# Kernel optimization log

Hardware: AMD Instinct MI355X
Metric: run time of the kernel (lower is better)

The kernel has to match this reference:

```python
import jax, jax.numpy as jnp
import numpy as np

DIM = 768
HEADS = 12
K_PARTS = 64
MLP_HIDDEN = 4 * DIM
EPS = 1e-5


def layer_norm(x, g, b):
    mu = jnp.mean(x, axis=-1, keepdims=True)
    var = jnp.mean(jnp.square(x - mu), axis=-1, keepdims=True)
    return (x - mu) * jax.lax.rsqrt(var + EPS) * g + b


def attention(x, qkv_w, qkv_b, proj_w, proj_b, num_heads):
    B, N, C = x.shape
    hd = C // num_heads
    scale = hd ** -0.5
    qkv = x @ qkv_w.T + qkv_b                      # (B,N,3C)
    qkv = qkv.reshape(B, N, 3, num_heads, hd).transpose(2, 0, 3, 1, 4)  # (3,B,H,N,hd)
    q, k, v = qkv[0], qkv[1], qkv[2]
    attn = jax.nn.softmax(jnp.einsum('bhqd,bhkd->bhqk', q, k) * scale, axis=-1)
    out = jnp.einsum('bhqk,bhkd->bhqd', attn, v)   # (B,H,N,hd)
    out = out.transpose(0, 2, 1, 3).reshape(B, N, C)
    return out @ proj_w.T + proj_b, attn


def mlp(x, fc1_w, fc1_b, fc2_w, fc2_b):
    h = jax.nn.gelu(x @ fc1_w.T + fc1_b, approximate=False)
    return h @ fc2_w.T + fc2_b


def setup_inputs() -> dict:
    key = jax.random.key(0)
    ks = jax.random.split(key, 16)
    s = lambda fan_in: 1.0 / np.sqrt(fan_in)
    inp = {
        'x': jax.random.normal(ks[0], (8, 1024, DIM), dtype=jnp.float32),
        'ln1_g': jnp.ones((DIM,), jnp.float32),
        'ln1_b': jnp.zeros((DIM,), jnp.float32),
        'qkv_w': jax.random.normal(ks[1], (3 * DIM, DIM), jnp.float32) * s(DIM),
        'qkv_b': jnp.zeros((3 * DIM,), jnp.float32),
        'proj_w': jax.random.normal(ks[2], (DIM, DIM), jnp.float32) * s(DIM),
        'proj_b': jnp.zeros((DIM,), jnp.float32),
        'c_qkv_w': jax.random.normal(ks[3], (3 * DIM, DIM), jnp.float32) * s(DIM),
        'c_qkv_b': jnp.zeros((3 * DIM,), jnp.float32),
        'c_proj_w': jax.random.normal(ks[4], (DIM, DIM), jnp.float32) * s(DIM),
        'c_proj_b': jnp.zeros((DIM,), jnp.float32),
        'cp_fc1_w': jax.random.normal(ks[5], (K_PARTS, K_PARTS), jnp.float32) * s(K_PARTS),
        'cp_fc1_b': jnp.zeros((K_PARTS,), jnp.float32),
        'cp_fc2_w': jax.random.normal(ks[6], (DIM, K_PARTS), jnp.float32) * s(K_PARTS),
        'cp_fc2_b': jnp.zeros((DIM,), jnp.float32),
        'P': jax.random.normal(ks[7], (K_PARTS, DIM), jnp.float32),
        'ln2_g': jnp.ones((DIM,), jnp.float32),
        'ln2_b': jnp.zeros((DIM,), jnp.float32),
        'fc1_w': jax.random.normal(ks[8], (MLP_HIDDEN, DIM), jnp.float32) * s(DIM),
        'fc1_b': jnp.zeros((MLP_HIDDEN,), jnp.float32),
        'fc2_w': jax.random.normal(ks[9], (DIM, MLP_HIDDEN), jnp.float32) * s(MLP_HIDDEN),
        'fc2_b': jnp.zeros((DIM,), jnp.float32),
    }
    # normalize P rows like the module init (F.normalize(orthogonal, dim=-1))
    inp['P'] = inp['P'] / jnp.linalg.norm(inp['P'], axis=-1, keepdims=True)
    return inp


def reference(x, ln1_g, ln1_b, qkv_w, qkv_b, proj_w, proj_b,
              c_qkv_w, c_qkv_b, c_proj_w, c_proj_b,
              cp_fc1_w, cp_fc1_b, cp_fc2_w, cp_fc2_b, P,
              ln2_g, ln2_b, fc1_w, fc1_b, fc2_w, fc2_b):
    n1 = layer_norm(x, ln1_g, ln1_b)
    y, _ = attention(n1, qkv_w, qkv_b, proj_w, proj_b, HEADS)
    # SimilarityMaps: L2-normalize tokens and parts, cosine similarity map (B,N,K)
    Un = n1 / jnp.linalg.norm(n1, axis=-1, keepdims=True)
    Pn = P / jnp.linalg.norm(P, axis=-1, keepdims=True)
    dmap = jnp.einsum('bnd,kd->bnk', Un, Pn)
    # c_project: Mlp K -> K -> dim, then parts attention
    zin = mlp(dmap, cp_fc1_w, cp_fc1_b, cp_fc2_w, cp_fc2_b)
    z, _ = attention(zin, c_qkv_w, c_qkv_b, c_proj_w, c_proj_b, HEADS)
    x = x + y + z                                  # gamma_1 is None, drop_path=0
    x = x + mlp(layer_norm(x, ln2_g, ln2_b), fc1_w, fc1_b, fc2_w, fc2_b)
    return x, dmap
```

## Files before the change

### kernel.cpp

```cpp
#include <hip/hip_runtime.h>


typedef unsigned short u16;
typedef unsigned int   u32;
typedef __attribute__((ext_vector_type(8))) short short8;
typedef __attribute__((ext_vector_type(8))) unsigned short ushort8v;
typedef __attribute__((ext_vector_type(4))) float f32x4;

#define F_GELU     1
#define F_ROWSCALE 2
#define F_RES1     4
#define F_RESF     8
#define F_OUTB     16
#define F_OUTF     32
#define F_BIAS     64

__device__ __forceinline__ float bf2f(u32 b) { return __uint_as_float(b << 16); }
__device__ __forceinline__ u16 f2bf(float f) {
    u32 u = __float_as_uint(f);
    u32 r = u + 0x7fffu + ((u >> 16) & 1u);
    return (u16)(r >> 16);
}
__device__ __forceinline__ u16 f2bf_fast(float f) {
    return (u16)((__float_as_uint(f) + 0x8000u) >> 16);
}
__device__ __forceinline__ float gelu_exact(float v) {
    return 0.5f * v * (1.0f + erff(v * 0.70710678118654752440f));
}
__device__ __forceinline__ float gelu_fast(float x) {
    float u = 0.79788456080286535588f * (x + 0.044715f * x * x * x);
    float e = __builtin_amdgcn_exp2f(u * 2.88539008177792681472f);
    float t = 1.0f - 2.0f / (e + 1.0f);
    return 0.5f * x * (1.0f + t);
}

__device__ __forceinline__ void gload16(const u16* g, u16* l) {
    __builtin_amdgcn_global_load_lds(
        (const __attribute__((address_space(1))) u32*)g,
        (__attribute__((address_space(3))) u32*)l, 16, 0, 0);
}

__global__ __launch_bounds__(256)
void conv_k(const float* __restrict__ src, u16* __restrict__ dst, int n)
{
    const int base = (blockIdx.x * 256 + threadIdx.x) * 4;
    if (base >= n) return;
    float4 v = *(const float4*)(src + base);
    ushort4 o;
    o.x = f2bf(v.x); o.y = f2bf(v.y); o.z = f2bf(v.z); o.w = f2bf(v.w);
    *(ushort4*)(dst + base) = o;
}

__device__ __forceinline__ float block_sum(float v, float* red) {
    #pragma unroll
    for (int off = 32; off > 0; off >>= 1) v += __shfl_down(v, off);
    __syncthreads();
    if ((threadIdx.x & 63) == 0) red[threadIdx.x >> 6] = v;
    __syncthreads();
    return red[0] + red[1] + red[2] + red[3];
}

template<bool NORM>
__global__ __launch_bounds__(256)
void ln_k(const float* __restrict__ xin, const float* __restrict__ g,
          const float* __restrict__ bta, u16* __restrict__ out,
          float* __restrict__ invnorm)
{
    __shared__ float red[4];
    const int row = blockIdx.x, t = threadIdx.x;
    float v[3];
    #pragma unroll
    for (int i = 0; i < 3; i++)
        v[i] = xin[(size_t)row * 768 + t + i * 256];
    float tot = block_sum(v[0] + v[1] + v[2], red);
    float mu  = tot * (1.0f / 768.0f);
    float d0 = v[0] - mu, d1 = v[1] - mu, d2 = v[2] - mu;
    float tot2 = block_sum(d0 * d0 + d1 * d1 + d2 * d2, red);
    float rstd = rsqrtf(tot2 * (1.0f / 768.0f) + 1e-5f);
    float ss = 0.0f;
    #pragma unroll
    for (int i = 0; i < 3; i++) {
        int c = t + i * 256;
        float yy = (v[i] - mu) * rstd * g[c] + bta[c];
        out[(size_t)row * 768 + c] = f2bf(yy);
        ss += yy * yy;
    }
    if constexpr (NORM) {
        float tot3 = block_sum(ss, red);
        if (t == 0) invnorm[row] = rsqrtf(tot3);
    }
}

__global__ __launch_bounds__(256)
void pn_k(const float* __restrict__ P, u16* __restrict__ Pn)
{
    __shared__ float red[4];
    const int row = blockIdx.x, t = threadIdx.x;
    float v[3];
    #pragma unroll
    for (int i = 0; i < 3; i++)
        v[i] = P[(size_t)row * 768 + t + i * 256];
    float tot = block_sum(v[0]*v[0] + v[1]*v[1] + v[2]*v[2], red);
    float inv = rsqrtf(tot);
    #pragma unroll
    for (int i = 0; i < 3; i++)
        Pn[(size_t)row * 768 + t + i * 256] = f2bf(v[i] * inv);
}

template<int FLAGS>
__global__ __launch_bounds__(256)
void gemm_mfma(const u16* __restrict__ A, const u16* __restrict__ W,
               const float* __restrict__ bias,
               const u16* __restrict__ res1, const float* __restrict__ resf,
               u16* __restrict__ out, float* __restrict__ outf,
               int M, int N, int K)
{
    __shared__ u16 smem[3][8192];
    const int t = threadIdx.x;
    const int wave = t >> 6, lane = t & 63;
    const int nbx  = gridDim.x;
    const int orig = blockIdx.x + blockIdx.y * nbx;
    const int cpx  = (nbx * gridDim.y) >> 3;
    const int wg   = (orig & 7) * cpx + (orig >> 3);
    const int m0 = (wg / nbx) * 128, n0 = (wg % nbx) * 128;
    const int Wm = (wave >> 1) * 64, Wn = (wave & 1) * 64;
    const int rr = lane >> 2, cc = (lane & 3) * 8;
    const int quad = lane >> 4, r16 = lane & 15;
    const int NK = K >> 5;

    f32x4 acc[4][4];
    #pragma unroll
    for (int i = 0; i < 4; i++)
        #pragma unroll
        for (int j = 0; j < 4; j++)
            acc[i][j] = (f32x4){0.f, 0.f, 0.f, 0.f};

    #pragma unroll
    for (int c = 0; c < 2; c++) {
        const int chunk = wave * 2 + c;
        const int row = chunk * 16 + rr;
        gload16(A + (size_t)(m0 + row) * K + cc, &smem[0][chunk * 512]);
        gload16(W + (size_t)(n0 + row) * K + cc, &smem[0][4096 + chunk * 512]);
    }
    if (NK > 1) {
        #pragma unroll
        for (int c = 0; c < 2; c++) {
            const int chunk = wave * 2 + c;
            const int row = chunk * 16 + rr;
            gload16(A + (size_t)(m0 + row) * K + 32 + cc, &smem[1][chunk * 512]);
            gload16(W + (size_t)(n0 + row) * K + 32 + cc, &smem[1][4096 + chunk * 512]);
        }
    }

    for (int kt = 0; kt < NK; kt++) {
        const int cur = kt % 3;
        if (kt + 2 < NK) {
            const int k0 = (kt + 2) * 32;
            const int nb = (kt + 2) % 3;
            #pragma unroll
            for (int c = 0; c < 2; c++) {
                const int chunk = wave * 2 + c;
                const int row = chunk * 16 + rr;
                gload16(A + (size_t)(m0 + row) * K + k0 + cc,
                        &smem[nb][chunk * 512]);
                gload16(W + (size_t)(n0 + row) * K + k0 + cc,
                        &smem[nb][4096 + chunk * 512]);
            }
            asm volatile("s_waitcnt vmcnt(8)\n\ts_barrier" ::: "memory");
        } else if (kt + 1 < NK) {
            asm volatile("s_waitcnt vmcnt(4)\n\ts_barrier" ::: "memory");
        } else {
            asm volatile("s_waitcnt vmcnt(0)\n\ts_barrier" ::: "memory");
        }
        short8 af[4], bfr[4];
        #pragma unroll
        for (int i = 0; i < 4; i++) {
            af[i]  = *(const short8*)&smem[cur][(Wm + i * 16 + r16) * 32 + quad * 8];
            bfr[i] = *(const short8*)&smem[cur][4096 + (Wn + i * 16 + r16) * 32 + quad * 8];
        }
        #pragma unroll
        for (int i = 0; i < 4; i++)
            #pragma unroll
            for (int j = 0; j < 4; j++)
                acc[i][j] = __builtin_amdgcn_mfma_f32_16x16x32_bf16(
                    af[i], bfr[j], acc[i][j], 0, 0, 0);
        asm volatile("s_barrier" ::: "memory");
    }

    float* myl = (float*)&smem[0][0] + wave * 1088;
    float bj[4];
    #pragma unroll
    for (int j = 0; j < 4; j++) {
        if constexpr (FLAGS & F_BIAS) bj[j] = bias[n0 + Wn + j * 16 + r16];
        else bj[j] = 0.0f;
    }
    const int row = lane >> 2, seg = (lane & 3) * 16;

    #pragma unroll
    for (int i = 0; i < 4; i++) {
        #pragma unroll
        for (int j = 0; j < 4; j++)
            #pragma unroll
            for (int r = 0; r < 4; r++) {
                float v = acc[i][j][r] + bj[j];
                if constexpr (FLAGS & F_GELU) v = gelu_fast(v);
                myl[(quad * 4 + r) * 68 + j * 16 + r16] = v;
            }
        float v[16];
        #pragma unroll
        for (int k4 = 0; k4 < 4; k4++) {
            float4 f = *(const float4*)&myl[row * 68 + seg + k4 * 4];
            v[k4 * 4 + 0] = f.x; v[k4 * 4 + 1] = f.y;
            v[k4 * 4 + 2] = f.z; v[k4 * 4 + 3] = f.w;
        }
        const int m = m0 + Wm + i * 16 + row;
        const size_t idx = (size_t)m * N + n0 + Wn + seg;
        if constexpr (FLAGS & F_RES1) {
            ushort8v r0 = *(const ushort8v*)(res1 + idx);
            ushort8v r1 = *(const ushort8v*)(res1 + idx + 8);
            #pragma unroll
            for (int k = 0; k < 8; k++) { v[k] += bf2f(r0[k]); v[k + 8] += bf2f(r1[k]); }
        }
        if constexpr (FLAGS & F_RESF) {
            #pragma unroll
            for (int k4 = 0; k4 < 4; k4++) {
                float4 f = *(const float4*)(resf + idx + k4 * 4);
                v[k4 * 4 + 0] += f.x; v[k4 * 4 + 1] += f.y;
                v[k4 * 4 + 2] += f.z; v[k4 * 4 + 3] += f.w;
            }
        }
        if constexpr (FLAGS & F_OUTB) {
            ushort8v o0, o1;
            #pragma unroll
            for (int k = 0; k < 8; k++) { o0[k] = f2bf(v[k]); o1[k] = f2bf(v[k + 8]); }
            *(ushort8v*)(out + idx) = o0;
            *(ushort8v*)(out + idx + 8) = o1;
        }
        if constexpr (FLAGS & F_OUTF) {
            #pragma unroll
            for (int k4 = 0; k4 < 4; k4++) {
                float4 f = {v[k4 * 4 + 0], v[k4 * 4 + 1], v[k4 * 4 + 2], v[k4 * 4 + 3]};
                *(float4*)(outf + idx + k4 * 4) = f;
            }
        }
    }
}

template<int BM, int BN, int FLAGS>
__global__ __launch_bounds__(256)
void gemm_k(const u16* __restrict__ A, const u16* __restrict__ W,
            const float* __restrict__ bias, const float* __restrict__ rowscale,
            const u16* __restrict__ res1, const float* __restrict__ resf,
            u16* __restrict__ out, float* __restrict__ outf,
            int M, int N, int K)
{
    constexpr int RM = BM / 16, RN = BN / 16;
    __shared__ float Asm[16][BM + 4];
    __shared__ float Wsm[16][BN + 4];
    const int t  = threadIdx.x;
    const int tx = t & 15, ty = t >> 4;
    const int m0 = blockIdx.y * BM, n0 = blockIdx.x * BN;

    float acc[RM][RN];
    #pragma unroll
    for (int i = 0; i < RM; i++)
        #pragma unroll
        for (int j = 0; j < RN; j++) acc[i][j] = 0.0f;

    for (int k0 = 0; k0 < K; k0 += 16) {
        #pragma unroll
        for (int i = 0; i < BM / 64; i++) {
            int f = t + i * 256, r = f >> 2, c4 = (f & 3) << 2;
            uint2 u = *(const uint2*)(A + (size_t)(m0 + r) * K + k0 + c4);
            Asm[c4 + 0][r] = bf2f(u.x & 0xffffu);
            Asm[c4 + 1][r] = bf2f(u.x >> 16);
            Asm[c4 + 2][r] = bf2f(u.y & 0xffffu);
            Asm[c4 + 3][r] = bf2f(u.y >> 16);
        }
        #pragma unroll
        for (int i = 0; i < BN / 64; i++) {
            int f = t + i * 256, r = f >> 2, c4 = (f & 3) << 2;
            uint2 u = *(const uint2*)(W + (size_t)(n0 + r) * K + k0 + c4);
            Wsm[c4 + 0][r] = bf2f(u.x & 0xffffu);
            Wsm[c4 + 1][r] = bf2f(u.x >> 16);
            Wsm[c4 + 2][r] = bf2f(u.y & 0xffffu);
            Wsm[c4 + 3][r] = bf2f(u.y >> 16);
        }
        __syncthreads();
        #pragma unroll
        for (int k = 0; k < 16; k++) {
            float a[RM], w[RN];
            #pragma unroll
            for (int ii = 0; ii < RM; ii += 4) {
                float4 v = *(const float4*)&Asm[k][ty * RM + ii];
                a[ii] = v.x; a[ii + 1] = v.y; a[ii + 2] = v.z; a[ii + 3] = v.w;
            }
            #pragma unroll
            for (int jj = 0; jj < RN; jj += 4) {
                float4 v = *(const float4*)&Wsm[k][tx * RN + jj];
                w[jj] = v.x; w[jj + 1] = v.y; w[jj + 2] = v.z; w[jj + 3] = v.w;
            }
            #pragma unroll
            for (int i = 0; i < RM; i++)
                #pragma unroll
                for (int j = 0; j < RN; j++)
                    acc[i][j] = fmaf(a[i], w[j], acc[i][j]);
        }
        __syncthreads();
    }

    #pragma unroll
    for (int i = 0; i < RM; i++) {
        const int m = m0 + ty * RM + i;
        float rs = 1.0f;
        if constexpr (FLAGS & F_ROWSCALE) rs = rowscale[m];
        #pragma unroll
        for (int jj = 0; jj < RN; jj += 4) {
            const int n = n0 + tx * RN + jj;
            const size_t idx = (size_t)m * N + n;
            float b4[4] = {0.f, 0.f, 0.f, 0.f};
            if constexpr (FLAGS & F_BIAS) {
                float4 bvv = *(const float4*)(bias + n);
                b4[0] = bvv.x; b4[1] = bvv.y; b4[2] = bvv.z; b4[3] = bvv.w;
            }
            float e[4];
            #pragma unroll
            for (int j = 0; j < 4; j++) {
                float v = acc[i][jj + j];
                if constexpr (FLAGS & F_BIAS) v += b4[j];
                if constexpr (FLAGS & F_GELU) v = gelu_exact(v);
                if constexpr (FLAGS & F_ROWSCALE) v *= rs;
                e[j] = v;
            }
            if constexpr (FLAGS & F_OUTB) {
                ushort4 o4;
                o4.x = f2bf(e[0]); o4.y = f2bf(e[1]);
                o4.z = f2bf(e[2]); o4.w = f2bf(e[3]);
                *(ushort4*)(out + idx) = o4;
            }
            if constexpr (FLAGS & F_OUTF) {
                float4 o4 = {e[0], e[1], e[2], e[3]};
                *(float4*)(outf + idx) = o4;
            }
        }
    }
}

__global__ __launch_bounds__(256)
void attn_mfma(const u16* __restrict__ qkv, u16* __restrict__ out)
{
    const int orig = blockIdx.x + blockIdx.y * 8;
    const int wg   = (orig & 7) * 96 + (orig >> 3);
    const int qt = wg & 7;
    const int bh = wg >> 3;
    const int b = bh / 12, h = bh % 12;
    __shared__ u16 Qs[2 * 128 * 32];
    __shared__ u16 Ks[2 * 64 * 32];
    __shared__ u16 Vt[2 * 64 * 32];
    __shared__ u16 Ps[2 * 128 * 32];
    const int t = threadIdx.x;
    const int wave = t >> 6, lane = t & 63;
    const int quad = lane >> 4, r16 = lane & 15;
    const size_t RS = 2304;
    const int tok0 = b * 1024 + qt * 128;
    const u16* qbase = qkv + (size_t)tok0 * RS + h * 64;
    const float SC = 0.125f * 1.44269504088896340736f;

    #pragma unroll
    for (int c = 0; c < 4; c++) {
        int idx = wave * 4 + c;
        int kc = idx >> 3, rg = idx & 7;
        int row = rg * 16 + (lane >> 2);
        gload16(qbase + (size_t)row * RS + kc * 32 + (lane & 3) * 8,
                &Qs[kc * 4096 + rg * 512]);
    }

    f32x4 O[2][4];
    float lpart[2][4];
    #pragma unroll
    for (int i = 0; i < 2; i++)
        #pragma unroll
        for (int j = 0; j < 4; j++) {
            O[i][j] = (f32x4){0.f, 0.f, 0.f, 0.f};
            lpart[i][j & 3] = 0.0f;
        }

    for (int kt = 0; kt < 16; kt++) {
        const u16* kbase = qkv + (size_t)(b * 1024 + kt * 64) * RS + 768 + h * 64;
        #pragma unroll
        for (int c = 0; c < 2; c++) {
            int idx = wave * 2 + c;
            int kc = idx >> 2, rg = idx & 3;
            int row = rg * 16 + (lane >> 2);
            gload16(kbase + (size_t)row * RS + kc * 32 + (lane & 3) * 8,
                    &Ks[kc * 2048 + rg * 512]);
        }
        const u16* vbase = qkv + (size_t)(b * 1024 + kt * 64) * RS + 1536 + h * 64;
        {
            const int kp = t & 63, dg = t >> 6;
            const int vb = (kp >> 5) * 2048 + (kp & 31);
            #pragma unroll
            for (int it = 0; it < 4; it++) {
                int d0 = dg * 16 + it * 4;
                uint2 u = *(const uint2*)(vbase + (size_t)kp * RS + d0);
                Vt[vb + (d0 + 0) * 32] = (u16)(u.x & 0xffffu);
                Vt[vb + (d0 + 1) * 32] = (u16)(u.x >> 16);
                Vt[vb + (d0 + 2) * 32] = (u16)(u.y & 0xffffu);
                Vt[vb + (d0 + 3) * 32] = (u16)(u.y >> 16);
            }
        }
        __syncthreads();

        f32x4 S[2][4];
        #pragma unroll
        for (int i = 0; i < 2; i++)
            #pragma unroll
            for (int j = 0; j < 4; j++)
                S[i][j] = (f32x4){0.f, 0.f, 0.f, 0.f};
        __builtin_amdgcn_s_setprio(1);
        #pragma unroll
        for (int kc = 0; kc < 2; kc++) {
            short8 aq[2], bk[4];
            #pragma unroll
            for (int i = 0; i < 2; i++)
                aq[i] = *(const short8*)&Qs[kc * 4096 + (wave * 32 + i * 16 + r16) * 32 + quad * 8];
            #pragma unroll
            for (int j = 0; j < 4; j++)
                bk[j] = *(const short8*)&Ks[kc * 2048 + (j * 16 + r16) * 32 + quad * 8];
            #pragma unroll
            for (int i = 0; i < 2; i++)
                #pragma unroll
                for (int j = 0; j < 4; j++)
                    S[i][j] = __builtin_amdgcn_mfma_f32_16x16x32_bf16(
                        aq[i], bk[j], S[i][j], 0, 0, 0);
        }
        __builtin_amdgcn_s_setprio(0);

        #pragma unroll
        for (int i = 0; i < 2; i++) {
            #pragma unroll
            for (int j = 0; j < 4; j++) {
                const int col = j * 16 + r16;
                const int pb = (col >> 5) * 4096 + (col & 31);
                #pragma unroll
                for (int r = 0; r < 4; r++) {
                    float p = __builtin_amdgcn_exp2f(S[i][j][r] * SC);
                    lpart[i][r] += p;
                    const int row = wave * 32 + i * 16 + quad * 4 + r;
                    Ps[pb + row * 32] = f2bf_fast(p);
                }
            }
        }

        __builtin_amdgcn_s_setprio(1);
        #pragma unroll
        for (int kc = 0; kc < 2; kc++) {
            short8 ap[2], bv[4];
            #pragma unroll
            for (int i = 0; i < 2; i++)
                ap[i] = *(const short8*)&Ps[kc * 4096 + (wave * 32 + i * 16 + r16) * 32 + quad * 8];
            #pragma unroll
            for (int j = 0; j < 4; j++)
                bv[j] = *(const short8*)&Vt[kc * 2048 + (j * 16 + r16) * 32 + quad * 8];
            #pragma unroll
            for (int i = 0; i < 2; i++)
                #pragma unroll
                for (int j = 0; j < 4; j++)
                    O[i][j] = __builtin_amdgcn_mfma_f32_16x16x32_bf16(
                        ap[i], bv[j], O[i][j], 0, 0, 0);
        }
        __builtin_amdgcn_s_setprio(0);
        __syncthreads();
    }

    const int row = lane >> 2, seg = (lane & 3) * 16;
    #pragma unroll
    for (int i = 0; i < 2; i++) {
        float linv[4];
        #pragma unroll
        for (int r = 0; r < 4; r++) {
            float l = lpart[i][r];
            l += __shfl_xor(l, 1);
            l += __shfl_xor(l, 2);
            l += __shfl_xor(l, 4);
            l += __shfl_xor(l, 8);
            linv[r] = 1.0f / l;
        }
        u16* myl = &Ps[wave * 2048 + i * 1024];
        #pragma unroll
        for (int j = 0; j < 4; j++)
            #pragma unroll
            for (int r = 0; r < 4; r++)
                myl[(quad * 4 + r) * 64 + j * 16 + r16] = f2bf(O[i][j][r] * linv[r]);
        const int token = tok0 + wave * 32 + i * 16 + row;
        const size_t oidx = (size_t)token * 768 + h * 64 + seg;
        *(ushort8v*)(out + oidx)     = *(const ushort8v*)&myl[row * 64 + seg];
        *(ushort8v*)(out + oidx + 8) = *(const ushort8v*)&myl[row * 64 + seg + 8];
    }
}

extern "C" void kernel_launch(void* const* d_in, const int* in_sizes, int n_in,
                              void* d_out, int out_size, void* d_ws, size_t ws_size,
                              hipStream_t stream)
{
    (void)in_sizes; (void)n_in; (void)out_size; (void)ws_size;
    const float* x        = (const float*)d_in[0];
    const float* ln1_g    = (const float*)d_in[1];
    const float* ln1_b    = (const float*)d_in[2];
    const float* qkv_w    = (const float*)d_in[3];
    const float* qkv_b    = (const float*)d_in[4];
    const float* proj_w   = (const float*)d_in[5];
    const float* proj_b   = (const float*)d_in[6];
    const float* c_qkv_w  = (const float*)d_in[7];
    const float* c_qkv_b  = (const float*)d_in[8];
    const float* c_proj_w = (const float*)d_in[9];
    const float* c_proj_b = (const float*)d_in[10];
    const float* cp_fc1_w = (const float*)d_in[11];
    const float* cp_fc1_b = (const float*)d_in[12];
    const float* cp_fc2_w = (const float*)d_in[13];
    const float* cp_fc2_b = (const float*)d_in[14];
    const float* P        = (const float*)d_in[15];
    const float* ln2_g    = (const float*)d_in[16];
    const float* ln2_b    = (const float*)d_in[17];
    const float* fc1_w    = (const float*)d_in[18];
    const float* fc1_b    = (const float*)d_in[19];
    const float* fc2_w    = (const float*)d_in[20];
    const float* fc2_b    = (const float*)d_in[21];

    float* out_x    = (float*)d_out;
    float* out_dmap = out_x + 6291456;

    u16* us    = (u16*)d_ws;
    u16* n1n2  = us;
    u16* bigA  = us + 6291456;
    u16* ao    = bigA + 18874368;
    u16* y     = us + 31457280;
    float* xs  = (float*)(us + 37748736);
    u16* dmapb = us + 50331648;
    u16* cph   = us + 50855936;
    u16* Pn    = us + 51380224;
    float* invn = (float*)(us + 51429376);
    u16* ci    = us + 51445760;

    u16* w_qkv   = ci;
    u16* w_proj  = ci + 1769472;
    u16* w_cqkv  = ci + 2359296;
    u16* w_cproj = ci + 4128768;
    u16* w_cpf1  = ci + 4718592;
    u16* w_cpf2  = ci + 4722688;
    u16* w_fc1   = ci + 4771840;
    u16* w_fc2   = ci + 7131136;

    const float* wsrc[8] = { qkv_w, proj_w, c_qkv_w, c_proj_w,
                             cp_fc1_w, cp_fc2_w, fc1_w, fc2_w };
    u16* wdst[8] = { w_qkv, w_proj, w_cqkv, w_cproj,
                     w_cpf1, w_cpf2, w_fc1, w_fc2 };
    const int wn[8] = { 1769472, 589824, 1769472, 589824,
                        4096, 49152, 2359296, 2359296 };
    for (int i = 0; i < 8; i++)
        conv_k<<<(wn[i] / 4 + 255) / 256, 256, 0, stream>>>(wsrc[i], wdst[i], wn[i]);

    pn_k<<<64, 256, 0, stream>>>(P, Pn);
    ln_k<true><<<8192, 256, 0, stream>>>(x, ln1_g, ln1_b, n1n2, invn);
    gemm_mfma<F_BIAS | F_OUTB>
        <<<dim3(18, 64), 256, 0, stream>>>(n1n2, w_qkv, qkv_b, nullptr, nullptr,
                                           bigA, nullptr, 8192, 2304, 768);
    attn_mfma<<<dim3(8, 96), 256, 0, stream>>>(bigA, ao);
    gemm_mfma<F_BIAS | F_OUTB>
        <<<dim3(6, 64), 256, 0, stream>>>(ao, w_proj, proj_b, nullptr, nullptr,
                                          y, nullptr, 8192, 768, 768);
    gemm_k<64, 64, F_ROWSCALE | F_OUTB | F_OUTF>
        <<<dim3(1, 128), 256, 0, stream>>>(n1n2, Pn, nullptr, invn, nullptr,
                                           nullptr, dmapb, out_dmap, 8192, 64, 768);
    gemm_k<64, 64, F_BIAS | F_GELU | F_OUTB>
        <<<dim3(1, 128), 256, 0, stream>>>(dmapb, w_cpf1, cp_fc1_b, nullptr,
                                           nullptr, nullptr, cph, nullptr, 8192, 64, 64);
    gemm_mfma<F_BIAS | F_OUTB>
        <<<dim3(6, 64), 256, 0, stream>>>(cph, w_cpf2, cp_fc2_b, nullptr, nullptr,
                                          n1n2, nullptr, 8192, 768, 64);
    gemm_mfma<F_BIAS | F_OUTB>
        <<<dim3(18, 64), 256, 0, stream>>>(n1n2, w_cqkv, c_qkv_b, nullptr, nullptr,
                                           bigA, nullptr, 8192, 2304, 768);
    attn_mfma<<<dim3(8, 96), 256, 0, stream>>>(bigA, ao);
    gemm_mfma<F_BIAS | F_RES1 | F_RESF | F_OUTF>
        <<<dim3(6, 64), 256, 0, stream>>>(ao, w_cproj, c_proj_b, y, x,
                                          nullptr, xs, 8192, 768, 768);
    ln_k<false><<<8192, 256, 0, stream>>>(xs, ln2_g, ln2_b, n1n2, nullptr);
    gemm_mfma<F_BIAS | F_GELU | F_OUTB>
        <<<dim3(24, 64), 256, 0, stream>>>(n1n2, w_fc1, fc1_b, nullptr, nullptr,
                                           bigA, nullptr, 8192, 3072, 768);
    gemm_mfma<F_BIAS | F_RESF | F_OUTF>
        <<<dim3(6, 64), 256, 0, stream>>>(bigA, w_fc2, fc2_b, nullptr, xs,
                                          nullptr, out_x, 8192, 768, 3072);
}
```

Baseline: 563.0 us.

## Prefetch next K/V tile during attention and regroup GEMM tile swizzle per XCD

In the attention kernel, the K tile for the next step is issued as an async global-to-LDS load after the softmax stage, and the V tile is loaded into registers. The V transpose into LDS moves to the start of the next iteration, so global latency overlaps with the P·V MFMAs instead of sitting before each S computation. The GEMM block-to-tile mapping changes so that each XCD gets a contiguous band of rows, walked in groups of six columns, to improve L2 reuse of A and W tiles. This costs extra registers for the V prefetch and assumes the grid dimensions divide evenly into the six-column groups.

```diff
diff --git a/kernel.cpp b/kernel.cpp
--- a/kernel.cpp
+++ b/kernel.cpp
@@ -121,8 +121,14 @@
     const int nbx  = gridDim.x;
     const int orig = blockIdx.x + blockIdx.y * nbx;
     const int cpx  = (nbx * gridDim.y) >> 3;
-    const int wg   = (orig & 7) * cpx + (orig >> 3);
-    const int m0 = (wg / nbx) * 128, n0 = (wg % nbx) * 128;
+    const int xcd  = orig & 7, loc = orig >> 3;
+    const int Rc   = cpx / nbx;
+    const int gsz  = 6 * Rc;
+    const int grp  = loc / gsz;
+    const int rem  = loc - grp * gsz;
+    const int ccol = grp * 6 + rem % 6;
+    const int crow = xcd * Rc + rem / 6;
+    const int m0 = crow * 128, n0 = ccol * 128;
     const int Wm = (wave >> 1) * 64, Wn = (wave & 1) * 64;
     const int rr = lane >> 2, cc = (lane & 3) * 8;
     const int quad = lane >> 4, r16 = lane & 15;
@@ -385,8 +391,12 @@
             lpart[i][j & 3] = 0.0f;
         }
 
-    for (int kt = 0; kt < 16; kt++) {
-        const u16* kbase = qkv + (size_t)(b * 1024 + kt * 64) * RS + 768 + h * 64;
+    const int kp = t & 63, dg = t >> 6;
+    const int vb = (kp >> 5) * 2048 + (kp & 31);
+    uint2 vr[4];
+
+    {
+        const u16* kbase = qkv + (size_t)(b * 1024) * RS + 768 + h * 64;
         #pragma unroll
         for (int c = 0; c < 2; c++) {
             int idx = wave * 2 + c;
@@ -395,21 +405,25 @@
             gload16(kbase + (size_t)row * RS + kc * 32 + (lane & 3) * 8,
                     &Ks[kc * 2048 + rg * 512]);
         }
-        const u16* vbase = qkv + (size_t)(b * 1024 + kt * 64) * RS + 1536 + h * 64;
-        {
-            const int kp = t & 63, dg = t >> 6;
-            const int vb = (kp >> 5) * 2048 + (kp & 31);
-            #pragma unroll
-            for (int it = 0; it < 4; it++) {
-                int d0 = dg * 16 + it * 4;
-                uint2 u = *(const uint2*)(vbase + (size_t)kp * RS + d0);
-                Vt[vb + (d0 + 0) * 32] = (u16)(u.x & 0xffffu);
-                Vt[vb + (d0 + 1) * 32] = (u16)(u.x >> 16);
-                Vt[vb + (d0 + 2) * 32] = (u16)(u.y & 0xffffu);
-                Vt[vb + (d0 + 3) * 32] = (u16)(u.y >> 16);
-            }
-        }
+        const u16* vbase = qkv + (size_t)(b * 1024) * RS + 1536 + h * 64;
+        #pragma unroll
+        for (int it = 0; it < 4; it++) {
+            int d0 = dg * 16 + it * 4;
+            vr[it] = *(const uint2*)(vbase + (size_t)kp * RS + d0);
+        }
+    }
+
+    for (int kt = 0; kt < 16; kt++) {
         __syncthreads();
+        #pragma unroll
+        for (int it = 0; it < 4; it++) {
+            int d0 = dg * 16 + it * 4;
+            uint2 u = vr[it];
+            Vt[vb + (d0 + 0) * 32] = (u16)(u.x & 0xffffu);
+            Vt[vb + (d0 + 1) * 32] = (u16)(u.x >> 16);
+            Vt[vb + (d0 + 2) * 32] = (u16)(u.y & 0xffffu);
+            Vt[vb + (d0 + 3) * 32] = (u16)(u.y >> 16);
+        }
 
         f32x4 S[2][4];
         #pragma unroll
@@ -452,6 +466,26 @@
             }
         }
 
+        __syncthreads();
+
+        if (kt < 15) {
+            const u16* kbase = qkv + (size_t)(b * 1024 + (kt + 1) * 64) * RS + 768 + h * 64;
+            #pragma unroll
+            for (int c = 0; c < 2; c++) {
+                int idx = wave * 2 + c;
+                int kc = idx >> 2, rg = idx & 3;
+                int row = rg * 16 + (lane >> 2);
+                gload16(kbase + (size_t)row * RS + kc * 32 + (lane & 3) * 8,
+                        &Ks[kc * 2048 + rg * 512]);
+            }
+            const u16* vbase = qkv + (size_t)(b * 1024 + (kt + 1) * 64) * RS + 1536 + h * 64;
+            #pragma unroll
+            for (int it = 0; it < 4; it++) {
+                int d0 = dg * 16 + it * 4;
+                vr[it] = *(const uint2*)(vbase + (size_t)kp * RS + d0);
+            }
+        }
+
         __builtin_amdgcn_s_setprio(1);
         #pragma unroll
         for (int kc = 0; kc < 2; kc++) {
@@ -470,7 +504,6 @@
                         ap[i], bv[j], O[i][j], 0, 0, 0);
         }
         __builtin_amdgcn_s_setprio(0);
-        __syncthreads();
     }
 
     const int row = lane >> 2, seg = (lane & 3) * 16;
```

Result: no change. 562.6 us (-0.1%).
